# Kernel tuning notes

Hardware: AMD Instinct MI355X
Metric: run time of the kernel (lower is better)

Reference implementation:

```python
import jax, jax.numpy as jnp
import numpy as np

B, S, D = 4, 2048, 1024
H, HD = 16, 64
MLP = 4 * D
EPS = 1e-6


def _rms_norm(x, scale):
    var = jnp.mean(jnp.square(x), axis=-1, keepdims=True)
    return x * jax.lax.rsqrt(var + EPS) * scale


def setup_inputs() -> dict:
    key = jax.random.key(0)
    ks = jax.random.split(key, 8)
    sd = D ** -0.5
    return {
        "x": jax.random.normal(ks[0], (B, S, D), jnp.float32),
        "pre_norm_scale": jnp.ones((D,), jnp.float32),
        "w_mlp_in": jax.random.normal(ks[1], (D, MLP), jnp.float32) * sd,   # MLPBlockInput, no bias
        "wq": jax.random.normal(ks[2], (D, H, HD), jnp.float32) * sd,
        "wk": jax.random.normal(ks[3], (D, H, HD), jnp.float32) * sd,
        "wv": jax.random.normal(ks[4], (D, H, HD), jnp.float32) * sd,
        "w_mlp_out": jax.random.normal(ks[5], (MLP, D), jnp.float32) * (MLP ** -0.5),
        "b_mlp_out": jnp.zeros((D,), jnp.float32),
        "w_attn_out": jax.random.normal(ks[6], (H, HD, D), jnp.float32) * sd,  # DenseGeneral axis=(-2,-1)
        "b_attn_out": jnp.zeros((D,), jnp.float32),
    }


def reference(x, pre_norm_scale, w_mlp_in, wq, wk, wv, w_mlp_out, b_mlp_out,
              w_attn_out, b_attn_out):
    residual = x
    xn = _rms_norm(x, pre_norm_scale)                      # pre_norm (TPNorm)

    # QKVMLPDense: fused MLP-input + QKV projections
    h = jax.nn.gelu(jnp.einsum("bsd,df->bsf", xn, w_mlp_in))   # [B,S,MLP]
    q = jnp.einsum("bsd,dhk->bshk", xn, wq)                    # [B,S,H,HD]
    k = jnp.einsum("bsd,dhk->bshk", xn, wk)
    v = jnp.einsum("bsd,dhk->bshk", xn, wv)

    # dot_product_attention (mask=None)
    scores = jnp.einsum("bqhd,bkhd->bhqk", q, k) / jnp.sqrt(jnp.asarray(HD, x.dtype))
    probs = jax.nn.softmax(scores, axis=-1)
    attn_v = jnp.einsum("bhqk,bkhd->bqhd", probs, v)           # [B,S,H,HD]

    # AttnMLPOut: mlp_out + attn_out
    mlp_out = jnp.einsum("bsf,fd->bsd", h, w_mlp_out) + b_mlp_out
    attn_out = jnp.einsum("bqhk,hkd->bqd", attn_v, w_attn_out) + b_attn_out
    block_out = mlp_out + attn_out                              # dropout is identity (train=False)
    return residual + block_out
```

## Files before the change

kernel.cpp:

```cpp
#include <hip/hip_runtime.h>
#include <cstdint>
#include <cstddef>

typedef float floatx4 __attribute__((ext_vector_type(4)));
typedef short bf16x8 __attribute__((ext_vector_type(8)));

#define MFMA(a, b, c) __builtin_amdgcn_mfma_f32_16x16x32_bf16((a), (b), (c), 0, 0, 0)

__device__ __forceinline__ unsigned short f2bf(float f) {
  union { float f; unsigned int u; } v; v.f = f;
  unsigned int u = v.u;
  unsigned int r = (u + 0x7FFFu + ((u >> 16) & 1u)) >> 16;
  return (unsigned short)r;
}

__device__ __forceinline__ void gload_lds16(const unsigned short* g, unsigned short* s) {
  __builtin_amdgcn_global_load_lds(
      (const __attribute__((address_space(1))) unsigned int*)g,
      (__attribute__((address_space(3))) unsigned int*)s, 16, 0, 0);
}

__global__ __launch_bounds__(256) void transpose_cast(
    const float* __restrict__ src, unsigned short* __restrict__ dst, int R, int C) {
  __shared__ float tile[32][33];
  int bx = blockIdx.x, by = blockIdx.y;
  int tx = threadIdx.x & 31, ty = threadIdx.x >> 5;
#pragma unroll
  for (int i = 0; i < 4; i++) {
    int r = ty + i * 8;
    tile[r][tx] = src[(size_t)(by * 32 + r) * C + bx * 32 + tx];
  }
  __syncthreads();
#pragma unroll
  for (int i = 0; i < 4; i++) {
    int r = ty + i * 8;
    dst[(size_t)(bx * 32 + r) * R + by * 32 + tx] = f2bf(tile[tx][r]);
  }
}

__global__ __launch_bounds__(256) void rmsnorm_kernel(
    const float* __restrict__ x, const float* __restrict__ scale,
    unsigned short* __restrict__ xn) {
  int row = blockIdx.x;
  const float4 v = ((const float4*)(x + (size_t)row * 1024))[threadIdx.x];
  float ss = v.x * v.x + v.y * v.y + v.z * v.z + v.w * v.w;
#pragma unroll
  for (int off = 1; off < 64; off <<= 1) ss += __shfl_xor(ss, off, 64);
  __shared__ float ws4[4];
  if ((threadIdx.x & 63) == 0) ws4[threadIdx.x >> 6] = ss;
  __syncthreads();
  float tot = ws4[0] + ws4[1] + ws4[2] + ws4[3];
  float rs = rsqrtf(tot * (1.0f / 1024.0f) + 1e-6f);
  const float4 sc = ((const float4*)scale)[threadIdx.x];
  uint2 o;
  o.x = (unsigned)f2bf(v.x * rs * sc.x) | ((unsigned)f2bf(v.y * rs * sc.y) << 16);
  o.y = (unsigned)f2bf(v.z * rs * sc.z) | ((unsigned)f2bf(v.w * rs * sc.w) << 16);
  ((uint2*)(xn + (size_t)row * 1024))[threadIdx.x] = o;
}

template <int MODE>
__global__ __launch_bounds__(256, 2) void gemm_bt(
    const unsigned short* __restrict__ A, const unsigned short* __restrict__ BT,
    int M, int N, int K, void* __restrict__ outp,
    const float* __restrict__ bias, const float* __restrict__ resid) {
  __shared__ unsigned short As[128 * 32];
  __shared__ unsigned short Bs[128 * 32];
  int m0 = blockIdx.y * 128, n0 = blockIdx.x * 128;
  int t = threadIdx.x, lane = t & 63, wave = t >> 6;
  int l15 = lane & 15, quad = lane >> 4;
  int wm = (wave & 1) * 64, wn = (wave >> 1) * 64;

  floatx4 acc[4][4] = {};

  int off0 = wave * 1024 + lane * 8;
  int off1 = off0 + 512;
  int r0 = off0 >> 5, c0 = off0 & 31;
  const unsigned short* gA0 = A + (size_t)(m0 + r0) * K + c0;
  const unsigned short* gA1 = A + (size_t)(m0 + r0 + 16) * K + c0;
  const unsigned short* gB0 = BT + (size_t)(n0 + r0) * K + c0;
  const unsigned short* gB1 = BT + (size_t)(n0 + r0 + 16) * K + c0;
  unsigned short* sA0 = &As[off0];
  unsigned short* sA1 = &As[off1];
  unsigned short* sB0 = &Bs[off0];
  unsigned short* sB1 = &Bs[off1];

  for (int kt = 0; kt < K; kt += 32) {
    __syncthreads();
    gload_lds16(gA0 + kt, sA0);
    gload_lds16(gA1 + kt, sA1);
    gload_lds16(gB0 + kt, sB0);
    gload_lds16(gB1 + kt, sB1);
    __syncthreads();
    bf16x8 a[4], b[4];
#pragma unroll
    for (int im = 0; im < 4; im++)
      a[im] = *(const bf16x8*)&As[(wm + im * 16 + l15) * 32 + quad * 8];
#pragma unroll
    for (int in_ = 0; in_ < 4; in_++)
      b[in_] = *(const bf16x8*)&Bs[(wn + in_ * 16 + l15) * 32 + quad * 8];
#pragma unroll
    for (int im = 0; im < 4; im++)
#pragma unroll
      for (int in_ = 0; in_ < 4; in_++)
        acc[im][in_] = MFMA(a[im], b[in_], acc[im][in_]);
  }

#pragma unroll
  for (int im = 0; im < 4; im++) {
#pragma unroll
    for (int in_ = 0; in_ < 4; in_++) {
#pragma unroll
      for (int r = 0; r < 4; r++) {
        int row = m0 + wm + im * 16 + quad * 4 + r;
        int col = n0 + wn + in_ * 16 + l15;
        float v = acc[im][in_][r];
        if constexpr (MODE == 0) {
          float z = 0.7978845608028654f * (v + 0.044715f * v * v * v);
          float e = __expf(2.0f * z);
          float th = 1.0f - 2.0f / (e + 1.0f);
          ((unsigned short*)outp)[(size_t)row * N + col] = f2bf(0.5f * v * (1.0f + th));
        } else if constexpr (MODE == 1) {
          int b_ = row >> 11, s = row & 2047, h = col >> 6, hd = col & 63;
          ((unsigned short*)outp)[(((size_t)(b_ * 16 + h)) * 2048 + s) * 64 + hd] = f2bf(v);
        } else if constexpr (MODE == 2) {
          int b_ = row >> 11, s = row & 2047, h = col >> 6, hd = col & 63;
          ((unsigned short*)outp)[(((size_t)(b_ * 16 + h)) * 64 + hd) * 2048 + s] = f2bf(v);
        } else if constexpr (MODE == 3) {
          ((float*)outp)[(size_t)row * N + col] = v + bias[col];
        } else if constexpr (MODE == 4) {
          size_t idx = (size_t)row * N + col;
          ((float*)outp)[idx] += v + bias[col] + resid[idx];
        } else {
          int b_ = row >> 11, s = row & 2047, h = col >> 6, hd = col & 63;
          ((unsigned short*)outp)[(((size_t)(b_ * 16 + h)) * 2048 + s) * 64 + hd] = f2bf(v * 0.125f);
        }
      }
    }
  }
}

__global__ __launch_bounds__(256, 2) void flash_attn(
    const unsigned short* __restrict__ q_buf, const unsigned short* __restrict__ k_buf,
    const unsigned short* __restrict__ v_buf, unsigned short* __restrict__ av_buf) {
  constexpr int S = 2048, HD = 64;
  constexpr int LK = 72, LV = 72, LP = 68;
  __shared__ unsigned short Ks[64 * LK];
  __shared__ unsigned short Vs[64 * LV];
  __shared__ unsigned short Ps[4][32 * LP];
  int qb = blockIdx.x, bh = blockIdx.y;
  int t = threadIdx.x, lane = t & 63, wave = t >> 6;
  int l15 = lane & 15, quad = lane >> 4;

  const unsigned short* qp = q_buf + (size_t)bh * S * HD;
  const unsigned short* kp = k_buf + (size_t)bh * S * HD;
  const unsigned short* vp = v_buf + (size_t)bh * HD * S;

  int q0 = qb * 128 + wave * 32;
  bf16x8 aQ[2][2];
#pragma unroll
  for (int qf = 0; qf < 2; qf++) {
    aQ[qf][0] = *(const bf16x8*)&qp[(size_t)(q0 + qf * 16 + l15) * HD + quad * 8];
    aQ[qf][1] = *(const bf16x8*)&qp[(size_t)(q0 + qf * 16 + l15) * HD + 32 + quad * 8];
  }

  floatx4 acc_o[2][4] = {};
  float lrow[2][4] = {};

  int kr = t >> 3, kc = (t & 7) * 8;

  for (int kv = 0; kv < S; kv += 64) {
    __syncthreads();
#pragma unroll
    for (int i = 0; i < 2; i++) {
      int r = kr + 32 * i;
      *(uint4*)&Ks[r * LK + kc] = *(const uint4*)&kp[(size_t)(kv + r) * HD + kc];
      *(uint4*)&Vs[r * LV + kc] = *(const uint4*)&vp[(size_t)r * S + kv + kc];
    }
    __syncthreads();

    floatx4 z[2][4];
#pragma unroll
    for (int cg = 0; cg < 4; cg++) {
      bf16x8 bk0 = *(const bf16x8*)&Ks[(cg * 16 + l15) * LK + quad * 8];
      bf16x8 bk1 = *(const bf16x8*)&Ks[(cg * 16 + l15) * LK + 32 + quad * 8];
#pragma unroll
      for (int qf = 0; qf < 2; qf++) {
        floatx4 acc = {};
        acc = MFMA(aQ[qf][0], bk0, acc);
        acc = MFMA(aQ[qf][1], bk1, acc);
        z[qf][cg] = acc;
      }
    }
#pragma unroll
    for (int qf = 0; qf < 2; qf++)
#pragma unroll
      for (int cg = 0; cg < 4; cg++)
#pragma unroll
        for (int r = 0; r < 4; r++) {
          float e = __expf(z[qf][cg][r]);
          lrow[qf][r] += e;
          Ps[wave][(qf * 16 + quad * 4 + r) * LP + cg * 16 + l15] = f2bf(e);
        }
    __syncthreads();
#pragma unroll
    for (int c = 0; c < 2; c++) {
      bf16x8 aP[2];
#pragma unroll
      for (int qf = 0; qf < 2; qf++) {
        const unsigned short* pp = &Ps[wave][(qf * 16 + l15) * LP + c * 32 + quad * 8];
        ((uint2*)&aP[qf])[0] = *(const uint2*)pp;
        ((uint2*)&aP[qf])[1] = *(const uint2*)(pp + 4);
      }
#pragma unroll
      for (int n = 0; n < 4; n++) {
        bf16x8 bv = *(const bf16x8*)&Vs[(n * 16 + l15) * LV + c * 32 + quad * 8];
        acc_o[0][n] = MFMA(aP[0], bv, acc_o[0][n]);
        acc_o[1][n] = MFMA(aP[1], bv, acc_o[1][n]);
      }
    }
  }

#pragma unroll
  for (int qf = 0; qf < 2; qf++)
#pragma unroll
    for (int r = 0; r < 4; r++) {
      float s = lrow[qf][r];
#pragma unroll
      for (int off = 1; off < 16; off <<= 1) s += __shfl_xor(s, off, 16);
      lrow[qf][r] = s;
    }

  int b_ = bh >> 4, h = bh & 15;
#pragma unroll
  for (int qf = 0; qf < 2; qf++)
#pragma unroll
    for (int r = 0; r < 4; r++) {
      float inv = 1.0f / lrow[qf][r];
      int srow = q0 + qf * 16 + quad * 4 + r;
      size_t base = ((size_t)(b_ * 2048 + srow)) * 1024 + h * 64;
#pragma unroll
      for (int n = 0; n < 4; n++)
        av_buf[base + n * 16 + l15] = f2bf(acc_o[qf][n][r] * inv);
    }
}

extern "C" void kernel_launch(void* const* d_in, const int* in_sizes, int n_in,
                              void* d_out, int out_size, void* d_ws, size_t ws_size,
                              hipStream_t stream) {
  (void)in_sizes; (void)n_in; (void)out_size; (void)ws_size;
  const float* x          = (const float*)d_in[0];
  const float* pns        = (const float*)d_in[1];
  const float* w_mlp_in   = (const float*)d_in[2];
  const float* wq         = (const float*)d_in[3];
  const float* wk         = (const float*)d_in[4];
  const float* wv         = (const float*)d_in[5];
  const float* w_mlp_out  = (const float*)d_in[6];
  const float* b_mlp_out  = (const float*)d_in[7];
  const float* w_attn_out = (const float*)d_in[8];
  const float* b_attn_out = (const float*)d_in[9];
  float* out = (float*)d_out;

  char* ws = (char*)d_ws;
  size_t off = 0;
  auto alloc = [&](size_t bytes) {
    void* p = ws + off;
    off += (bytes + 255) & ~(size_t)255;
    return p;
  };
  const size_t M = 8192;
  unsigned short* xn       = (unsigned short*)alloc(M * 1024 * 2);
  unsigned short* wmlpinT  = (unsigned short*)alloc((size_t)4096 * 1024 * 2);
  unsigned short* wqT      = (unsigned short*)alloc((size_t)1024 * 1024 * 2);
  unsigned short* wkT      = (unsigned short*)alloc((size_t)1024 * 1024 * 2);
  unsigned short* wvT      = (unsigned short*)alloc((size_t)1024 * 1024 * 2);
  unsigned short* wmlpoutT = (unsigned short*)alloc((size_t)1024 * 4096 * 2);
  unsigned short* wattnT   = (unsigned short*)alloc((size_t)1024 * 1024 * 2);
  unsigned short* hbuf     = (unsigned short*)alloc(M * 4096 * 2);
  unsigned short* qb       = (unsigned short*)alloc(M * 1024 * 2);
  unsigned short* kb       = (unsigned short*)alloc(M * 1024 * 2);
  unsigned short* vb       = (unsigned short*)alloc(M * 1024 * 2);
  unsigned short* avb      = (unsigned short*)alloc(M * 1024 * 2);

  transpose_cast<<<dim3(128, 32), 256, 0, stream>>>(w_mlp_in, wmlpinT, 1024, 4096);
  transpose_cast<<<dim3(32, 32), 256, 0, stream>>>(wq, wqT, 1024, 1024);
  transpose_cast<<<dim3(32, 32), 256, 0, stream>>>(wk, wkT, 1024, 1024);
  transpose_cast<<<dim3(32, 32), 256, 0, stream>>>(wv, wvT, 1024, 1024);
  transpose_cast<<<dim3(32, 128), 256, 0, stream>>>(w_mlp_out, wmlpoutT, 4096, 1024);
  transpose_cast<<<dim3(32, 32), 256, 0, stream>>>(w_attn_out, wattnT, 1024, 1024);

  rmsnorm_kernel<<<dim3(8192), 256, 0, stream>>>(x, pns, xn);

  gemm_bt<0><<<dim3(32, 64), 256, 0, stream>>>(xn, wmlpinT, 8192, 4096, 1024, hbuf, nullptr, nullptr);
  gemm_bt<5><<<dim3(8, 64), 256, 0, stream>>>(xn, wqT, 8192, 1024, 1024, qb, nullptr, nullptr);
  gemm_bt<1><<<dim3(8, 64), 256, 0, stream>>>(xn, wkT, 8192, 1024, 1024, kb, nullptr, nullptr);
  gemm_bt<2><<<dim3(8, 64), 256, 0, stream>>>(xn, wvT, 8192, 1024, 1024, vb, nullptr, nullptr);

  flash_attn<<<dim3(16, 64), 256, 0, stream>>>(qb, kb, vb, avb);

  gemm_bt<3><<<dim3(8, 64), 256, 0, stream>>>(avb, wattnT, 8192, 1024, 1024, out, b_attn_out, nullptr);
  gemm_bt<4><<<dim3(8, 64), 256, 0, stream>>>(hbuf, wmlpoutT, 8192, 1024, 4096, out, b_mlp_out, x);
}
```

Measured before the change: 563.2 us.

## Fuse MLP-in with QKV GEMMs and attn-out with MLP-out via concatenated weights

Concatenates the MLP-input and Q/K/V weights into one transposed matrix so a single GEMM produces the GELU hidden activations and the Q/K/V heads. Attention output is written into the same concatenated buffer next to the hidden activations, so one K=5120 GEMM computes mlp_out+attn_out+biases+residual without the read-modify-write of the output. Adds an XCD-aware block remapping for the GEMMs and flash attention to improve L2 locality. This cuts kernel launches, tail effects and the extra fp32 output traffic, at the cost of more complex index math and branching in the epilogue.

```diff
diff --git a/kernel.cpp b/kernel.cpp
--- a/kernel.cpp
+++ b/kernel.cpp
@@ -21,7 +21,8 @@
 }
 
 __global__ __launch_bounds__(256) void transpose_cast(
-    const float* __restrict__ src, unsigned short* __restrict__ dst, int R, int C) {
+    const float* __restrict__ src, unsigned short* __restrict__ dst,
+    int R, int C, int ldd) {
   __shared__ float tile[32][33];
   int bx = blockIdx.x, by = blockIdx.y;
   int tx = threadIdx.x & 31, ty = threadIdx.x >> 5;
@@ -34,7 +35,7 @@
 #pragma unroll
   for (int i = 0; i < 4; i++) {
     int r = ty + i * 8;
-    dst[(size_t)(bx * 32 + r) * R + by * 32 + tx] = f2bf(tile[tx][r]);
+    dst[(size_t)(bx * 32 + r) * ldd + by * 32 + tx] = f2bf(tile[tx][r]);
   }
 }
 
@@ -61,11 +62,22 @@
 template <int MODE>
 __global__ __launch_bounds__(256, 2) void gemm_bt(
     const unsigned short* __restrict__ A, const unsigned short* __restrict__ BT,
-    int M, int N, int K, void* __restrict__ outp,
-    const float* __restrict__ bias, const float* __restrict__ resid) {
+    int K, void* __restrict__ outp,
+    const float* __restrict__ bias1, const float* __restrict__ bias2,
+    const float* __restrict__ resid,
+    int msplit, int tm, int tn,
+    unsigned short* __restrict__ q_out, unsigned short* __restrict__ k_out,
+    unsigned short* __restrict__ v_out) {
   __shared__ unsigned short As[128 * 32];
   __shared__ unsigned short Bs[128 * 32];
-  int m0 = blockIdx.y * 128, n0 = blockIdx.x * 128;
+
+  int id = blockIdx.x + gridDim.x * blockIdx.y;
+  int xcd = id & 7, j = id >> 3;
+  int mh = xcd % msplit, nq = xcd / msplit;
+  int by = mh * tm + j / tn;
+  int bx = nq * tn + j % tn;
+  int m0 = by * 128, n0 = bx * 128;
+
   int t = threadIdx.x, lane = t & 63, wave = t >> 6;
   int l15 = lane & 15, quad = lane >> 4;
   int wm = (wave & 1) * 64, wn = (wave >> 1) * 64;
@@ -114,25 +126,26 @@
         int row = m0 + wm + im * 16 + quad * 4 + r;
         int col = n0 + wn + in_ * 16 + l15;
         float v = acc[im][in_][r];
-        if constexpr (MODE == 0) {
-          float z = 0.7978845608028654f * (v + 0.044715f * v * v * v);
-          float e = __expf(2.0f * z);
-          float th = 1.0f - 2.0f / (e + 1.0f);
-          ((unsigned short*)outp)[(size_t)row * N + col] = f2bf(0.5f * v * (1.0f + th));
-        } else if constexpr (MODE == 1) {
-          int b_ = row >> 11, s = row & 2047, h = col >> 6, hd = col & 63;
-          ((unsigned short*)outp)[(((size_t)(b_ * 16 + h)) * 2048 + s) * 64 + hd] = f2bf(v);
-        } else if constexpr (MODE == 2) {
-          int b_ = row >> 11, s = row & 2047, h = col >> 6, hd = col & 63;
-          ((unsigned short*)outp)[(((size_t)(b_ * 16 + h)) * 64 + hd) * 2048 + s] = f2bf(v);
-        } else if constexpr (MODE == 3) {
-          ((float*)outp)[(size_t)row * N + col] = v + bias[col];
-        } else if constexpr (MODE == 4) {
-          size_t idx = (size_t)row * N + col;
-          ((float*)outp)[idx] += v + bias[col] + resid[idx];
+        if constexpr (MODE == 6) {
+          if (n0 < 4096) {
+            float z = 0.7978845608028654f * (v + 0.044715f * v * v * v);
+            float e = __expf(2.0f * z);
+            float th = 1.0f - 2.0f / (e + 1.0f);
+            ((unsigned short*)outp)[(size_t)row * 5120 + col] = f2bf(0.5f * v * (1.0f + th));
+          } else {
+            int seg = (n0 - 4096) >> 10;
+            int cs = col - 4096 - (seg << 10);
+            int b_ = row >> 11, s = row & 2047, h = cs >> 6, hd = cs & 63;
+            if (seg == 0)
+              q_out[(((size_t)(b_ * 16 + h)) * 2048 + s) * 64 + hd] = f2bf(v * 0.125f);
+            else if (seg == 1)
+              k_out[(((size_t)(b_ * 16 + h)) * 2048 + s) * 64 + hd] = f2bf(v);
+            else
+              v_out[(((size_t)(b_ * 16 + h)) * 64 + hd) * 2048 + s] = f2bf(v);
+          }
         } else {
-          int b_ = row >> 11, s = row & 2047, h = col >> 6, hd = col & 63;
-          ((unsigned short*)outp)[(((size_t)(b_ * 16 + h)) * 2048 + s) * 64 + hd] = f2bf(v * 0.125f);
+          size_t idx = (size_t)row * 1024 + col;
+          ((float*)outp)[idx] = v + bias1[col] + bias2[col] + resid[idx];
         }
       }
     }
@@ -141,13 +154,18 @@
 
 __global__ __launch_bounds__(256, 2) void flash_attn(
     const unsigned short* __restrict__ q_buf, const unsigned short* __restrict__ k_buf,
-    const unsigned short* __restrict__ v_buf, unsigned short* __restrict__ av_buf) {
+    const unsigned short* __restrict__ v_buf, unsigned short* __restrict__ cat) {
   constexpr int S = 2048, HD = 64;
   constexpr int LK = 72, LV = 72, LP = 68;
   __shared__ unsigned short Ks[64 * LK];
   __shared__ unsigned short Vs[64 * LV];
   __shared__ unsigned short Ps[4][32 * LP];
-  int qb = blockIdx.x, bh = blockIdx.y;
+
+  int id = blockIdx.x + gridDim.x * blockIdx.y;
+  int xcd = id & 7, j = id >> 3;
+  int bh = xcd * 8 + (j >> 4);
+  int qbk = j & 15;
+
   int t = threadIdx.x, lane = t & 63, wave = t >> 6;
   int l15 = lane & 15, quad = lane >> 4;
 
@@ -155,7 +173,7 @@
   const unsigned short* kp = k_buf + (size_t)bh * S * HD;
   const unsigned short* vp = v_buf + (size_t)bh * HD * S;
 
-  int q0 = qb * 128 + wave * 32;
+  int q0 = qbk * 128 + wave * 32;
   bf16x8 aQ[2][2];
 #pragma unroll
   for (int qf = 0; qf < 2; qf++) {
@@ -237,10 +255,10 @@
     for (int r = 0; r < 4; r++) {
       float inv = 1.0f / lrow[qf][r];
       int srow = q0 + qf * 16 + quad * 4 + r;
-      size_t base = ((size_t)(b_ * 2048 + srow)) * 1024 + h * 64;
+      size_t base = ((size_t)(b_ * 2048 + srow)) * 5120 + 4096 + h * 64;
 #pragma unroll
       for (int n = 0; n < 4; n++)
-        av_buf[base + n * 16 + l15] = f2bf(acc_o[qf][n][r] * inv);
+        cat[base + n * 16 + l15] = f2bf(acc_o[qf][n][r] * inv);
     }
 }
 
@@ -268,35 +286,28 @@
     return p;
   };
   const size_t M = 8192;
-  unsigned short* xn       = (unsigned short*)alloc(M * 1024 * 2);
-  unsigned short* wmlpinT  = (unsigned short*)alloc((size_t)4096 * 1024 * 2);
-  unsigned short* wqT      = (unsigned short*)alloc((size_t)1024 * 1024 * 2);
-  unsigned short* wkT      = (unsigned short*)alloc((size_t)1024 * 1024 * 2);
-  unsigned short* wvT      = (unsigned short*)alloc((size_t)1024 * 1024 * 2);
-  unsigned short* wmlpoutT = (unsigned short*)alloc((size_t)1024 * 4096 * 2);
-  unsigned short* wattnT   = (unsigned short*)alloc((size_t)1024 * 1024 * 2);
-  unsigned short* hbuf     = (unsigned short*)alloc(M * 4096 * 2);
-  unsigned short* qb       = (unsigned short*)alloc(M * 1024 * 2);
-  unsigned short* kb       = (unsigned short*)alloc(M * 1024 * 2);
-  unsigned short* vb       = (unsigned short*)alloc(M * 1024 * 2);
-  unsigned short* avb      = (unsigned short*)alloc(M * 1024 * 2);
-
-  transpose_cast<<<dim3(128, 32), 256, 0, stream>>>(w_mlp_in, wmlpinT, 1024, 4096);
-  transpose_cast<<<dim3(32, 32), 256, 0, stream>>>(wq, wqT, 1024, 1024);
-  transpose_cast<<<dim3(32, 32), 256, 0, stream>>>(wk, wkT, 1024, 1024);
-  transpose_cast<<<dim3(32, 32), 256, 0, stream>>>(wv, wvT, 1024, 1024);
-  transpose_cast<<<dim3(32, 128), 256, 0, stream>>>(w_mlp_out, wmlpoutT, 4096, 1024);
-  transpose_cast<<<dim3(32, 32), 256, 0, stream>>>(w_attn_out, wattnT, 1024, 1024);
+  unsigned short* xn     = (unsigned short*)alloc(M * 1024 * 2);
+  unsigned short* wcatT  = (unsigned short*)alloc((size_t)7168 * 1024 * 2);
+  unsigned short* wcat2T = (unsigned short*)alloc((size_t)1024 * 5120 * 2);
+  unsigned short* cat    = (unsigned short*)alloc(M * 5120 * 2);
+  unsigned short* qb     = (unsigned short*)alloc(M * 1024 * 2);
+  unsigned short* kb     = (unsigned short*)alloc(M * 1024 * 2);
+  unsigned short* vb     = (unsigned short*)alloc(M * 1024 * 2);
+
+  transpose_cast<<<dim3(128, 32), 256, 0, stream>>>(w_mlp_in, wcatT, 1024, 4096, 1024);
+  transpose_cast<<<dim3(32, 32), 256, 0, stream>>>(wq, wcatT + (size_t)4096 * 1024, 1024, 1024, 1024);
+  transpose_cast<<<dim3(32, 32), 256, 0, stream>>>(wk, wcatT + (size_t)5120 * 1024, 1024, 1024, 1024);
+  transpose_cast<<<dim3(32, 32), 256, 0, stream>>>(wv, wcatT + (size_t)6144 * 1024, 1024, 1024, 1024);
+  transpose_cast<<<dim3(32, 128), 256, 0, stream>>>(w_mlp_out, wcat2T, 4096, 1024, 5120);
+  transpose_cast<<<dim3(32, 32), 256, 0, stream>>>(w_attn_out, wcat2T + 4096, 1024, 1024, 5120);
 
   rmsnorm_kernel<<<dim3(8192), 256, 0, stream>>>(x, pns, xn);
 
-  gemm_bt<0><<<dim3(32, 64), 256, 0, stream>>>(xn, wmlpinT, 8192, 4096, 1024, hbuf, nullptr, nullptr);
-  gemm_bt<5><<<dim3(8, 64), 256, 0, stream>>>(xn, wqT, 8192, 1024, 1024, qb, nullptr, nullptr);
-  gemm_bt<1><<<dim3(8, 64), 256, 0, stream>>>(xn, wkT, 8192, 1024, 1024, kb, nullptr, nullptr);
-  gemm_bt<2><<<dim3(8, 64), 256, 0, stream>>>(xn, wvT, 8192, 1024, 1024, vb, nullptr, nullptr);
-
-  flash_attn<<<dim3(16, 64), 256, 0, stream>>>(qb, kb, vb, avb);
-
-  gemm_bt<3><<<dim3(8, 64), 256, 0, stream>>>(avb, wattnT, 8192, 1024, 1024, out, b_attn_out, nullptr);
-  gemm_bt<4><<<dim3(8, 64), 256, 0, stream>>>(hbuf, wmlpoutT, 8192, 1024, 4096, out, b_mlp_out, x);
-}
+  gemm_bt<6><<<dim3(56, 64), 256, 0, stream>>>(
+      xn, wcatT, 1024, cat, nullptr, nullptr, nullptr, 2, 32, 14, qb, kb, vb);
+
+  flash_attn<<<dim3(16, 64), 256, 0, stream>>>(qb, kb, vb, cat);
+
+  gemm_bt<7><<<dim3(8, 64), 256, 0, stream>>>(
+      cat, wcat2T, 5120, out, b_mlp_out, b_attn_out, x, 8, 8, 8, nullptr, nullptr, nullptr);
+}
```

Result: no change. 554.1 us (-1.6%).
